# Performance work log

Hardware: AMD Instinct MI355X
Metric: run time of the kernel (lower is better)

Reference implementation:

```python
import jax, jax.numpy as jnp
import numpy as np
import math

B, S, E, H = 2, 2048, 1024, 16
HD = E // H          # head_dim = 64
HX = 64              # helix_dim
P = HX // 2          # helix pairs = 32

def setup_inputs() -> dict:
    key = jax.random.key(0)
    ks = jax.random.split(key, 12)
    sc = 0.02
    return {
        "x":    jax.random.normal(ks[0], (B, S, E), dtype=jnp.float32),
        "Wq":   jax.random.normal(ks[1], (E, E), dtype=jnp.float32) * sc,
        "bq":   jnp.zeros((E,), dtype=jnp.float32),
        "Wk":   jax.random.normal(ks[2], (E, E), dtype=jnp.float32) * sc,
        "bk":   jnp.zeros((E,), dtype=jnp.float32),
        "Wv":   jax.random.normal(ks[3], (E, E), dtype=jnp.float32) * sc,
        "bv":   jnp.zeros((E,), dtype=jnp.float32),
        "Wo":   jax.random.normal(ks[4], (E, E), dtype=jnp.float32) * sc,
        "bo":   jnp.zeros((E,), dtype=jnp.float32),
        "Whel": jax.random.normal(ks[5], (H, HX, HD), dtype=jnp.float32) * sc,
        "bhel": jnp.zeros((H, HX), dtype=jnp.float32),
    }

def _l2norm(x, eps=1e-12):
    # torch F.normalize(p=2, dim=-1): x / max(||x||, eps)
    n = jnp.sqrt(jnp.sum(x * x, axis=-1, keepdims=True))
    return x / jnp.maximum(n, eps)

def _scramble(t):
    # faithful to torch: (B,S,2) -> transpose(1,2) -> reshape(B,S,2),
    # vectorized over (H,P): t is (B,H,P,S,2)
    b, h, p, s, _ = t.shape
    return jnp.swapaxes(t, -1, -2).reshape(b, h, p, s, 2)

def reference(x, Wq, bq, Wk, bk, Wv, bv, Wo, bo, Whel, bhel):
    b, s, e = x.shape
    h, hx, hd = Whel.shape
    p = hx // 2
    q = x @ Wq.T + bq
    k = x @ Wk.T + bk
    v = x @ Wv.T + bv
    qh = q.reshape(b, s, h, hd)
    kh = k.reshape(b, s, h, hd)
    # per-head helical projections: (B,S,H,HX)
    q_hel = jnp.einsum('bshd,hed->bshe', qh, Whel) + bhel
    k_hel = jnp.einsum('bshd,hed->bshe', kh, Whel) + bhel
    # split into 2D coords, normalize each pair: (B,H,P,S,2)
    qn = _l2norm(q_hel.reshape(b, s, h, p, 2)).transpose(0, 2, 3, 1, 4)
    kn = _l2norm(k_hel.reshape(b, s, h, p, 2)).transpose(0, 2, 3, 1, 4)
    qn = _scramble(qn)
    kn = _scramble(kn)
    # helical similarity averaged over pairs: (B,H,S,S)
    helical = jnp.einsum('bhpsc,bhptc->bhst', qn, kn) / p
    # standard scaled dot-product scores
    dot = jnp.einsum('bshd,bthd->bhst', qh, kh) / math.sqrt(hd)
    alpha = 0.5
    attn = jax.nn.softmax(alpha * dot + (1.0 - alpha) * helical, axis=-1)
    vh = v.reshape(b, s, h, hd)
    out = jnp.einsum('bhst,bthd->bshd', attn, vh).reshape(b, s, e)
    return out @ Wo.T + bo
```

## Files before the change

### kernel.cpp

```cpp
#include <hip/hip_runtime.h>
#include <hip/hip_bf16.h>


typedef unsigned short u16;
typedef unsigned int u32;
typedef __attribute__((ext_vector_type(8))) __bf16 bf16x8;
typedef __attribute__((ext_vector_type(4))) float f32x4;
typedef __attribute__((ext_vector_type(16))) float f32x16;

union BFrag { u32 u[4]; bf16x8 b; };

__device__ __forceinline__ u16 f2b(float f) {
  u32 u = __float_as_uint(f);
  u32 r = (u + 0x7fffu + ((u >> 16) & 1u)) >> 16;
  return (u16)r;
}
__device__ __forceinline__ float b2f(u16 h) {
  return __uint_as_float(((u32)h) << 16);
}

__device__ __forceinline__ f32x4 mfma16(bf16x8 a, bf16x8 b, f32x4 c) {
  return __builtin_amdgcn_mfma_f32_16x16x32_bf16(a, b, c, 0, 0, 0);
}
__device__ __forceinline__ f32x16 mfma32(bf16x8 a, bf16x8 b, f32x16 c) {
  return __builtin_amdgcn_mfma_f32_32x32x16_bf16(a, b, c, 0, 0, 0);
}

__device__ __forceinline__ void gld16(void* lds, const void* g) {
  __builtin_amdgcn_global_load_lds(
      (const __attribute__((address_space(1))) unsigned int*)g,
      (__attribute__((address_space(3))) unsigned int*)lds, 16, 0, 0);
}

__device__ __forceinline__ void pl32swap(u32& a, u32& b, int l5) {
#if __has_builtin(__builtin_amdgcn_permlane32_swap)
  typedef unsigned int u32x2v __attribute__((ext_vector_type(2)));
  u32x2v r = __builtin_amdgcn_permlane32_swap(a, b, false, false);
  a = r[0];
  b = r[1];
#else
  u32 ea = __shfl_xor((int)a, 32);
  u32 eb = __shfl_xor((int)b, 32);
  u32 na = l5 ? eb : a;
  u32 nb = l5 ? b : ea;
  a = na;
  b = nb;
#endif
}

#define LOG2E 1.4426950408889634f

__global__ __launch_bounds__(256) void cast_kernel(
    const float* __restrict__ x,  const float* __restrict__ wq,
    const float* __restrict__ wk, const float* __restrict__ wv,
    const float* __restrict__ wo, const float* __restrict__ whel,
    u16* __restrict__ xb, u16* __restrict__ wb, u16* __restrict__ wob,
    u16* __restrict__ whb) {
  long long q = (long long)blockIdx.x * 256 + threadIdx.x;
  const float* s; u16* d; long long base;
  if (q < 1048576)      { s = x;    d = xb;            base = 0; }
  else if (q < 1310720) { s = wq;   d = wb;            base = 1048576; }
  else if (q < 1572864) { s = wk;   d = wb + 1048576;  base = 1310720; }
  else if (q < 1835008) { s = wv;   d = wb + 2097152;  base = 1572864; }
  else if (q < 2097152) { s = wo;   d = wob;           base = 1835008; }
  else                  { s = whel; d = whb;           base = 2097152; }
  long long e = (q - base) * 4;
  float4 v = *(const float4*)(s + e);
  ushort4 o;
  o.x = f2b(v.x); o.y = f2b(v.y); o.z = f2b(v.z); o.w = f2b(v.w);
  *(ushort4*)(d + e) = o;
}

__global__ __launch_bounds__(256, 3) void qkv_gemm(
    const u16* __restrict__ xb, const u16* __restrict__ wb,
    const float* __restrict__ bq, const float* __restrict__ bk,
    const float* __restrict__ bv, const u16* __restrict__ whb,
    const float* __restrict__ bhel,
    u16* __restrict__ Qcat, u16* __restrict__ Kcat, u16* __restrict__ vt) {
  union SM {
    struct { u16 Al[2][128][32]; u16 Bl[2][128][32]; u16 T[64][136]; } m;
    struct { u16 Th[4][32][72]; u16 Hs[2][128][64]; } e;
  };
  __shared__ SM sm;
  const int nt = blockIdx.x, mt = blockIdx.y;
  const int which = nt >> 3;
  const int n0 = (nt & 7) << 7;
  const int m0 = mt << 7;
  const int tid = threadIdx.x;
  const int wave = tid >> 6, lane = tid & 63;
  const int g = lane >> 4, c15 = lane & 15;
  const int wm = wave & 1, wn = wave >> 1;
  const u16* Wp = wb + (long long)which * (1024 * 1024) + n0 * 1024;
  const u16* Ap = xb + m0 * 1024;
  const int srow = (wave * 64 + lane) >> 2;
  const int scol = (lane & 3) << 3;

  f32x4 acc[4][4];
#pragma unroll
  for (int i = 0; i < 4; i++)
#pragma unroll
    for (int j = 0; j < 4; j++) acc[i][j] = f32x4{0.f, 0.f, 0.f, 0.f};

  gld16(&sm.m.Al[0][srow][scol],      Ap + srow * 1024 + scol);
  gld16(&sm.m.Al[0][64 + srow][scol], Ap + (64 + srow) * 1024 + scol);
  gld16(&sm.m.Bl[0][srow][scol],      Wp + srow * 1024 + scol);
  gld16(&sm.m.Bl[0][64 + srow][scol], Wp + (64 + srow) * 1024 + scol);

  for (int k0 = 0; k0 < 1024; k0 += 32) {
    const int c = (k0 >> 5) & 1;
    __syncthreads();
    if (k0 + 32 < 1024) {
      const int kn = k0 + 32;
      gld16(&sm.m.Al[c ^ 1][srow][scol],      Ap + srow * 1024 + kn + scol);
      gld16(&sm.m.Al[c ^ 1][64 + srow][scol],
            Ap + (64 + srow) * 1024 + kn + scol);
      gld16(&sm.m.Bl[c ^ 1][srow][scol],      Wp + srow * 1024 + kn + scol);
      gld16(&sm.m.Bl[c ^ 1][64 + srow][scol],
            Wp + (64 + srow) * 1024 + kn + scol);
    }
    bf16x8 a[4], b[4];
#pragma unroll
    for (int i = 0; i < 4; i++)
      a[i] = *(const bf16x8*)&sm.m.Al[c][wm * 64 + i * 16 + c15][g * 8];
#pragma unroll
    for (int j = 0; j < 4; j++)
      b[j] = *(const bf16x8*)&sm.m.Bl[c][wn * 64 + j * 16 + c15][g * 8];
#pragma unroll
    for (int i = 0; i < 4; i++)
#pragma unroll
      for (int j = 0; j < 4; j++) acc[i][j] = mfma16(a[i], b[j], acc[i][j]);
  }

  if (which == 2) {
#pragma unroll
    for (int half = 0; half < 2; ++half) {
      __syncthreads();
      if (wn == half) {
#pragma unroll
        for (int i = 0; i < 4; i++)
#pragma unroll
          for (int j = 0; j < 4; j++)
#pragma unroll
            for (int r = 0; r < 4; r++) {
              int nloc = j * 16 + c15;
              int mloc = wm * 64 + i * 16 + g * 4 + r;
              float v = acc[i][j][r] + bv[n0 + half * 64 + nloc];
              sm.m.T[nloc][mloc] = f2b(v);
            }
      }
      __syncthreads();
#pragma unroll
      for (int it = 0; it < 4; ++it) {
        int idx = it * 256 + tid;
        int row = idx >> 4;
        int cm = (idx & 15) * 8;
        int col = n0 + half * 64 + row;
        int hh = col >> 6, dd = col & 63;
        int m = m0 + cm;
        int bb2 = m >> 11, s = m & 2047;
        *(uint4*)&vt[(((bb2 * 16 + hh) * 64) + dd) * 2048 + s] =
            *(const uint4*)&sm.m.T[row][cm];
      }
    }
    return;
  }

  const float* bias = (which == 0) ? bq : bk;
  const float fold = (which == 0) ? (0.0625f * LOG2E) : 1.0f;
  const float osc  = (which == 0) ? (0.125f * LOG2E) : 0.125f;
  const int h0 = n0 >> 6;
  const int hsel = h0 + wn;
  u16* Dst = ((which == 0) ? Qcat : Kcat);

  bf16x8 wf[2][4];
#pragma unroll
  for (int kh = 0; kh < 2; ++kh)
#pragma unroll
    for (int nf = 0; nf < 4; ++nf)
      wf[kh][nf] = *(const bf16x8*)(whb + hsel * 4096 + (nf * 16 + c15) * 64 +
                                    kh * 32 + g * 8);

  __syncthreads();
  const int bb2 = m0 >> 11;
  const int ubase = (m0 & 2047) >> 1;

#pragma unroll
  for (int half = 0; half < 2; ++half) {
#pragma unroll
    for (int i2 = 0; i2 < 2; ++i2) {
      int i = half * 2 + i2;
#pragma unroll
      for (int j = 0; j < 4; ++j)
#pragma unroll
        for (int r = 0; r < 4; ++r) {
          int row = m0 + wm * 64 + i * 16 + g * 4 + r;
          int col = n0 + wn * 64 + j * 16 + c15;
          float vraw = acc[i][j][r] + bias[col];
          int bb = row >> 11, s = row & 2047;
          int d = col & 63;
          Dst[(((long long)(bb * 16 + hsel) * 2048) + s) * 128 + d] =
              f2b(vraw * fold);
          sm.e.Th[wave][i2 * 16 + g * 4 + r][j * 16 + c15] = f2b(vraw);
        }
    }
    f32x4 hacc[2][4];
#pragma unroll
    for (int mf = 0; mf < 2; ++mf)
#pragma unroll
      for (int nf = 0; nf < 4; ++nf) hacc[mf][nf] = f32x4{0.f, 0.f, 0.f, 0.f};
#pragma unroll
    for (int kh = 0; kh < 2; ++kh) {
      bf16x8 a0 = *(const bf16x8*)&sm.e.Th[wave][c15][kh * 32 + g * 8];
      bf16x8 a1 = *(const bf16x8*)&sm.e.Th[wave][16 + c15][kh * 32 + g * 8];
#pragma unroll
      for (int nf = 0; nf < 4; ++nf) {
        hacc[0][nf] = mfma16(a0, wf[kh][nf], hacc[0][nf]);
        hacc[1][nf] = mfma16(a1, wf[kh][nf], hacc[1][nf]);
      }
    }
#pragma unroll
    for (int mf = 0; mf < 2; ++mf)
#pragma unroll
      for (int nf = 0; nf < 4; ++nf)
#pragma unroll
        for (int r = 0; r < 4; ++r) {
          int e = nf * 16 + c15;
          float v = hacc[mf][nf][r] + bhel[hsel * 64 + e];
          float pp = __shfl_xor(v, 1);
          float nn = sqrtf(v * v + pp * pp);
          float o = v / fmaxf(nn, 1e-12f) * osc;
          int tl = wm * 64 + half * 32 + mf * 16 + g * 4 + r;
          sm.e.Hs[wn][(e & 1) * 64 + (tl >> 1)][(e & ~1) | (tl & 1)] = f2b(o);
        }
  }
  __syncthreads();
#pragma unroll
  for (int it = 0; it < 8; ++it) {
    int idx = it * 256 + tid;
    int hh = idx >> 10;
    int hr = (idx >> 3) & 127;
    int ck = idx & 7;
    int coord = hr >> 6, ul = hr & 63;
    int row_out = coord * 1024 + ubase + ul;
    *(uint4*)&Dst[(((long long)(bb2 * 16 + h0 + hh) * 2048) + row_out) * 128 +
                  64 + ck * 8] = *(const uint4*)&sm.e.Hs[hh][hr][ck * 8];
  }
}

__global__ __launch_bounds__(512, 4) void attn_kernel(
    const u16* __restrict__ Qcat, const u16* __restrict__ Kcat,
    const u16* __restrict__ vt, u16* __restrict__ AO) {
  __shared__ u16 Kl[2][64][128];
  __shared__ u16 Vl[2][64][64];
  __shared__ float denl[2][128];
  const int bh = blockIdx.x, qt = blockIdx.y;
  const int bb = bh >> 4, h = bh & 15;
  const int q0 = qt << 7;
  const int tid = threadIdx.x;
  const int w = tid >> 6, lane = tid & 63;
  const int wq = w & 3, wt = w >> 2;
  const int l31 = lane & 31, l5 = lane >> 5;
  const u16* Qb = Qcat + (long long)bh * (2048 * 128);
  const u16* Kb = Kcat + (long long)bh * (2048 * 128);
  const u16* Vb = vt + (long long)bh * (64 * 2048);

  bf16x8 qf[8];
  {
    const u16* qrow = Qb + (q0 + 32 * wq + l31) * 128 + l5 * 8;
#pragma unroll
    for (int ks = 0; ks < 8; ++ks) qf[ks] = *(const bf16x8*)(qrow + ks * 16);
  }

  const int ll = tid;
  const int krow0 = ll >> 4;
  const int kp = ll & 15;
  const int ksrc0 = (kp & 8) | ((kp & 7) ^ (krow0 & 7));
  const int krow1 = 32 + krow0;
  const int ksrc1 = (kp & 8) | ((kp & 7) ^ (krow1 & 7));
  const int vd = ll >> 3;
  const int vsrc = (ll & 7) ^ (vd & 7);

  gld16(((u16*)Kl[0]) + ll * 8,        Kb + krow0 * 128 + ksrc0 * 8);
  gld16(((u16*)Kl[0]) + 4096 + ll * 8, Kb + krow1 * 128 + ksrc1 * 8);
  gld16(((u16*)Vl[0]) + ll * 8,        Vb + vd * 2048 + vsrc * 8);

  f32x16 accO0, accO1;
#pragma unroll
  for (int i = 0; i < 16; ++i) { accO0[i] = 0.f; accO1[i] = 0.f; }
  float den = 0.f;

  const int krow = 32 * wt + l31;
  const int kr7 = krow & 7;

  for (int t = 0; t < 32; ++t) {
    const int cur = t & 1;
    __syncthreads();
    if (t + 1 < 32) {
      const int t1 = (t + 1) << 6;
      u16* Kd = (u16*)Kl[cur ^ 1];
      gld16(Kd + ll * 8,        Kb + (t1 + krow0) * 128 + ksrc0 * 8);
      gld16(Kd + 4096 + ll * 8, Kb + (t1 + krow1) * 128 + ksrc1 * 8);
      gld16(((u16*)Vl[cur ^ 1]) + ll * 8, Vb + vd * 2048 + t1 + vsrc * 8);
    }

    f32x16 accS;
#pragma unroll
    for (int i = 0; i < 16; ++i) accS[i] = 0.f;
#pragma unroll
    for (int ks = 0; ks < 8; ++ks) {
      int lc = 2 * ks + l5;
      int p = (lc & 8) | ((lc & 7) ^ kr7);
      bf16x8 ak = *(const bf16x8*)&Kl[cur][krow][p * 8];
      accS = mfma32(ak, qf[ks], accS);
    }

    u32 D0[2], D1[2], D2[2], D3[2];
#pragma unroll
    for (int rr = 0; rr < 4; ++rr) {
      float p0 = __builtin_amdgcn_exp2f(accS[4 * rr + 0]);
      float p1 = __builtin_amdgcn_exp2f(accS[4 * rr + 1]);
      float p2 = __builtin_amdgcn_exp2f(accS[4 * rr + 2]);
      float p3 = __builtin_amdgcn_exp2f(accS[4 * rr + 3]);
      den += (p0 + p1) + (p2 + p3);
      u32 lo = __builtin_amdgcn_perm(__float_as_uint(p1), __float_as_uint(p0),
                                     0x07060302u);
      u32 hi = __builtin_amdgcn_perm(__float_as_uint(p3), __float_as_uint(p2),
                                     0x07060302u);
      if (rr == 0) { D0[0] = lo; D0[1] = hi; }
      else if (rr == 1) { D1[0] = lo; D1[1] = hi; }
      else if (rr == 2) { D2[0] = lo; D2[1] = hi; }
      else { D3[0] = lo; D3[1] = hi; }
    }
    BFrag A0, A1;
    A0.u[0] = D0[0]; A0.u[2] = D1[0]; pl32swap(A0.u[0], A0.u[2], l5);
    A0.u[1] = D0[1]; A0.u[3] = D1[1]; pl32swap(A0.u[1], A0.u[3], l5);
    A1.u[0] = D2[0]; A1.u[2] = D3[0]; pl32swap(A1.u[0], A1.u[2], l5);
    A1.u[1] = D2[1]; A1.u[3] = D3[1]; pl32swap(A1.u[1], A1.u[3], l5);

#pragma unroll
    for (int dq = 0; dq < 2; ++dq) {
      int d = 32 * dq + l31;
      int d7 = d & 7;
#pragma unroll
      for (int ks = 0; ks < 2; ++ks) {
        int lc = 4 * wt + 2 * ks + l5;
        bf16x8 bvf = *(const bf16x8*)&Vl[cur][d][((lc ^ d7) & 7) * 8];
        if (dq == 0) accO0 = mfma32(ks ? A1.b : A0.b, bvf, accO0);
        else         accO1 = mfma32(ks ? A1.b : A0.b, bvf, accO1);
      }
    }
  }

  den += __shfl_xor(den, 32);
  if (lane < 32) denl[wt][32 * wq + lane] = den;
  __syncthreads();

  float* S = (float*)Kl;
  if (wt == 1) {
#pragma unroll
    for (int r = 0; r < 16; ++r) {
      int qr = (r & 3) + 8 * (r >> 2) + 4 * l5;
      S[(wq * 32 + qr) * 64 + l31] = accO0[r];
      S[(wq * 32 + qr) * 64 + 32 + l31] = accO1[r];
    }
  }
  __syncthreads();
  if (wt == 0) {
#pragma unroll
    for (int r = 0; r < 16; ++r) {
      int qr = (r & 3) + 8 * (r >> 2) + 4 * l5;
      int ql = 32 * wq + qr;
      float inv = 1.0f / (denl[0][ql] + denl[1][ql]);
      float o0 = (accO0[r] + S[(wq * 32 + qr) * 64 + l31]) * inv;
      float o1 = (accO1[r] + S[(wq * 32 + qr) * 64 + 32 + l31]) * inv;
      long long base = ((long long)(bb * 2048 + q0 + ql) * 1024) + h * 64;
      AO[base + l31] = f2b(o0);
      AO[base + 32 + l31] = f2b(o1);
    }
  }
}

__global__ __launch_bounds__(256, 2) void out_gemm(
    const u16* __restrict__ AO, const u16* __restrict__ wob,
    const float* __restrict__ bo, float* __restrict__ out) {
  __shared__ u16 Al[2][128][32];
  __shared__ u16 Bl[2][64][32];
  const int n0 = blockIdx.x << 6;
  const int m0 = blockIdx.y << 7;
  const int tid = threadIdx.x;
  const int wave = tid >> 6, lane = tid & 63;
  const int g = lane >> 4, c15 = lane & 15;
  const int wm = wave & 1, wn = wave >> 1;
  const u16* Wp = wob + n0 * 1024;
  const u16* Ap = AO + m0 * 1024;
  const int srow = tid >> 2;
  const int scol = (tid & 3) << 3;

  f32x4 acc[4][2];
#pragma unroll
  for (int i = 0; i < 4; i++)
#pragma unroll
    for (int j = 0; j < 2; j++) acc[i][j] = f32x4{0.f, 0.f, 0.f, 0.f};

  gld16(&Al[0][srow][scol],      Ap + srow * 1024 + scol);
  gld16(&Al[0][64 + srow][scol], Ap + (64 + srow) * 1024 + scol);
  gld16(&Bl[0][srow][scol],      Wp + srow * 1024 + scol);

  for (int k0 = 0; k0 < 1024; k0 += 32) {
    const int c = (k0 >> 5) & 1;
    __syncthreads();
    if (k0 + 32 < 1024) {
      const int kn = k0 + 32;
      gld16(&Al[c ^ 1][srow][scol],      Ap + srow * 1024 + kn + scol);
      gld16(&Al[c ^ 1][64 + srow][scol], Ap + (64 + srow) * 1024 + kn + scol);
      gld16(&Bl[c ^ 1][srow][scol],      Wp + srow * 1024 + kn + scol);
    }
    bf16x8 a[4], b[2];
#pragma unroll
    for (int i = 0; i < 4; i++)
      a[i] = *(const bf16x8*)&Al[c][wm * 64 + i * 16 + c15][g * 8];
#pragma unroll
    for (int j = 0; j < 2; j++)
      b[j] = *(const bf16x8*)&Bl[c][wn * 32 + j * 16 + c15][g * 8];
#pragma unroll
    for (int i = 0; i < 4; i++)
#pragma unroll
      for (int j = 0; j < 2; j++) acc[i][j] = mfma16(a[i], b[j], acc[i][j]);
  }
#pragma unroll
  for (int i = 0; i < 4; i++)
#pragma unroll
    for (int j = 0; j < 2; j++)
#pragma unroll
      for (int r = 0; r < 4; r++) {
        int row = m0 + wm * 64 + i * 16 + g * 4 + r;
        int col = n0 + wn * 32 + j * 16 + c15;
        out[row * 1024 + col] = acc[i][j][r] + bo[col];
      }
}

extern "C" void kernel_launch(void* const* d_in, const int* in_sizes, int n_in,
                              void* d_out, int out_size, void* d_ws,
                              size_t ws_size, hipStream_t stream) {
  const float* x    = (const float*)d_in[0];
  const float* Wq   = (const float*)d_in[1];
  const float* bq   = (const float*)d_in[2];
  const float* Wk   = (const float*)d_in[3];
  const float* bk   = (const float*)d_in[4];
  const float* Wv   = (const float*)d_in[5];
  const float* bv   = (const float*)d_in[6];
  const float* Wo   = (const float*)d_in[7];
  const float* bo   = (const float*)d_in[8];
  const float* Whel = (const float*)d_in[9];
  const float* bhel = (const float*)d_in[10];
  float* out = (float*)d_out;

  char* ws = (char*)d_ws;
  u16* xb   = (u16*)(ws + 0);
  u16* wb   = (u16*)(ws + 8388608);
  u16* wob  = (u16*)(ws + 14680064);
  u16* whb  = (u16*)(ws + 16777216);
  u16* Qcat = (u16*)(ws + 16908288);
  u16* Kcat = (u16*)(ws + 33685504);
  u16* vt   = (u16*)(ws + 50462720);
  u16* AO   = (u16*)(ws + 58851328);

  cast_kernel<<<dim3(8256), dim3(256), 0, stream>>>(x, Wq, Wk, Wv, Wo, Whel,
                                                    xb, wb, wob, whb);
  qkv_gemm<<<dim3(24, 32), dim3(256), 0, stream>>>(xb, wb, bq, bk, bv, whb,
                                                   bhel, Qcat, Kcat, vt);
  attn_kernel<<<dim3(32, 16), dim3(512), 0, stream>>>(Qcat, Kcat, vt, AO);
  out_gemm<<<dim3(16, 32), dim3(256), 0, stream>>>(AO, wob, bo, out);
}
```

Before: 228.7 us.

## Double query rows per attention block to reuse K/V tiles across two Q fragments

```diff
diff --git a/kernel.cpp b/kernel.cpp
--- a/kernel.cpp
+++ b/kernel.cpp
@@ -247,15 +247,15 @@
   }
 }
 
-__global__ __launch_bounds__(512, 4) void attn_kernel(
+__global__ __launch_bounds__(512, 2) void attn_kernel(
     const u16* __restrict__ Qcat, const u16* __restrict__ Kcat,
     const u16* __restrict__ vt, u16* __restrict__ AO) {
   __shared__ u16 Kl[2][64][128];
   __shared__ u16 Vl[2][64][64];
-  __shared__ float denl[2][128];
+  __shared__ float denl[2][256];
   const int bh = blockIdx.x, qt = blockIdx.y;
   const int bb = bh >> 4, h = bh & 15;
-  const int q0 = qt << 7;
+  const int q0 = qt << 8;
   const int tid = threadIdx.x;
   const int w = tid >> 6, lane = tid & 63;
   const int wq = w & 3, wt = w >> 2;
@@ -264,11 +264,15 @@
   const u16* Kb = Kcat + (long long)bh * (2048 * 128);
   const u16* Vb = vt + (long long)bh * (64 * 2048);
 
-  bf16x8 qf[8];
+  bf16x8 qf0[8], qf1[8];
   {
-    const u16* qrow = Qb + (q0 + 32 * wq + l31) * 128 + l5 * 8;
-#pragma unroll
-    for (int ks = 0; ks < 8; ++ks) qf[ks] = *(const bf16x8*)(qrow + ks * 16);
+    const u16* qrow0 = Qb + (q0 + 64 * wq + l31) * 128 + l5 * 8;
+    const u16* qrow1 = qrow0 + 32 * 128;
+#pragma unroll
+    for (int ks = 0; ks < 8; ++ks) {
+      qf0[ks] = *(const bf16x8*)(qrow0 + ks * 16);
+      qf1[ks] = *(const bf16x8*)(qrow1 + ks * 16);
+    }
   }
 
   const int ll = tid;
@@ -284,10 +288,12 @@
   gld16(((u16*)Kl[0]) + 4096 + ll * 8, Kb + krow1 * 128 + ksrc1 * 8);
   gld16(((u16*)Vl[0]) + ll * 8,        Vb + vd * 2048 + vsrc * 8);
 
-  f32x16 accO0, accO1;
-#pragma unroll
-  for (int i = 0; i < 16; ++i) { accO0[i] = 0.f; accO1[i] = 0.f; }
-  float den = 0.f;
+  f32x16 accO00, accO01, accO10, accO11;
+#pragma unroll
+  for (int i = 0; i < 16; ++i) {
+    accO00[i] = 0.f; accO01[i] = 0.f; accO10[i] = 0.f; accO11[i] = 0.f;
+  }
+  float den0 = 0.f, den1 = 0.f;
 
   const int krow = 32 * wt + l31;
   const int kr7 = krow & 7;
@@ -303,39 +309,65 @@
       gld16(((u16*)Vl[cur ^ 1]) + ll * 8, Vb + vd * 2048 + t1 + vsrc * 8);
     }
 
-    f32x16 accS;
-#pragma unroll
-    for (int i = 0; i < 16; ++i) accS[i] = 0.f;
+    f32x16 accS0, accS1;
+#pragma unroll
+    for (int i = 0; i < 16; ++i) { accS0[i] = 0.f; accS1[i] = 0.f; }
 #pragma unroll
     for (int ks = 0; ks < 8; ++ks) {
       int lc = 2 * ks + l5;
       int p = (lc & 8) | ((lc & 7) ^ kr7);
       bf16x8 ak = *(const bf16x8*)&Kl[cur][krow][p * 8];
-      accS = mfma32(ak, qf[ks], accS);
-    }
-
-    u32 D0[2], D1[2], D2[2], D3[2];
-#pragma unroll
-    for (int rr = 0; rr < 4; ++rr) {
-      float p0 = __builtin_amdgcn_exp2f(accS[4 * rr + 0]);
-      float p1 = __builtin_amdgcn_exp2f(accS[4 * rr + 1]);
-      float p2 = __builtin_amdgcn_exp2f(accS[4 * rr + 2]);
-      float p3 = __builtin_amdgcn_exp2f(accS[4 * rr + 3]);
-      den += (p0 + p1) + (p2 + p3);
-      u32 lo = __builtin_amdgcn_perm(__float_as_uint(p1), __float_as_uint(p0),
-                                     0x07060302u);
-      u32 hi = __builtin_amdgcn_perm(__float_as_uint(p3), __float_as_uint(p2),
-                                     0x07060302u);
-      if (rr == 0) { D0[0] = lo; D0[1] = hi; }
-      else if (rr == 1) { D1[0] = lo; D1[1] = hi; }
-      else if (rr == 2) { D2[0] = lo; D2[1] = hi; }
-      else { D3[0] = lo; D3[1] = hi; }
-    }
-    BFrag A0, A1;
-    A0.u[0] = D0[0]; A0.u[2] = D1[0]; pl32swap(A0.u[0], A0.u[2], l5);
-    A0.u[1] = D0[1]; A0.u[3] = D1[1]; pl32swap(A0.u[1], A0.u[3], l5);
-    A1.u[0] = D2[0]; A1.u[2] = D3[0]; pl32swap(A1.u[0], A1.u[2], l5);
-    A1.u[1] = D2[1]; A1.u[3] = D3[1]; pl32swap(A1.u[1], A1.u[3], l5);
+      accS0 = mfma32(ak, qf0[ks], accS0);
+      accS1 = mfma32(ak, qf1[ks], accS1);
+    }
+
+    BFrag A0q0, A1q0, A0q1, A1q1;
+    {
+      u32 D0[2], D1[2], D2[2], D3[2];
+#pragma unroll
+      for (int rr = 0; rr < 4; ++rr) {
+        float p0 = __builtin_amdgcn_exp2f(accS0[4 * rr + 0]);
+        float p1 = __builtin_amdgcn_exp2f(accS0[4 * rr + 1]);
+        float p2 = __builtin_amdgcn_exp2f(accS0[4 * rr + 2]);
+        float p3 = __builtin_amdgcn_exp2f(accS0[4 * rr + 3]);
+        den0 += (p0 + p1) + (p2 + p3);
+        u32 lo = __builtin_amdgcn_perm(__float_as_uint(p1),
+                                       __float_as_uint(p0), 0x07060302u);
+        u32 hi = __builtin_amdgcn_perm(__float_as_uint(p3),
+                                       __float_as_uint(p2), 0x07060302u);
+        if (rr == 0) { D0[0] = lo; D0[1] = hi; }
+        else if (rr == 1) { D1[0] = lo; D1[1] = hi; }
+        else if (rr == 2) { D2[0] = lo; D2[1] = hi; }
+        else { D3[0] = lo; D3[1] = hi; }
+      }
+      A0q0.u[0] = D0[0]; A0q0.u[2] = D1[0]; pl32swap(A0q0.u[0], A0q0.u[2], l5);
+      A0q0.u[1] = D0[1]; A0q0.u[3] = D1[1]; pl32swap(A0q0.u[1], A0q0.u[3], l5);
+      A1q0.u[0] = D2[0]; A1q0.u[2] = D3[0]; pl32swap(A1q0.u[0], A1q0.u[2], l5);
+      A1q0.u[1] = D2[1]; A1q0.u[3] = D3[1]; pl32swap(A1q0.u[1], A1q0.u[3], l5);
+    }
+    {
+      u32 D0[2], D1[2], D2[2], D3[2];
+#pragma unroll
+      for (int rr = 0; rr < 4; ++rr) {
+        float p0 = __builtin_amdgcn_exp2f(accS1[4 * rr + 0]);
+        float p1 = __builtin_amdgcn_exp2f(accS1[4 * rr + 1]);
+        float p2 = __builtin_amdgcn_exp2f(accS1[4 * rr + 2]);
+        float p3 = __builtin_amdgcn_exp2f(accS1[4 * rr + 3]);
+        den1 += (p0 + p1) + (p2 + p3);
+        u32 lo = __builtin_amdgcn_perm(__float_as_uint(p1),
+                                       __float_as_uint(p0), 0x07060302u);
+        u32 hi = __builtin_amdgcn_perm(__float_as_uint(p3),
+                                       __float_as_uint(p2), 0x07060302u);
+        if (rr == 0) { D0[0] = lo; D0[1] = hi; }
+        else if (rr == 1) { D1[0] = lo; D1[1] = hi; }
+        else if (rr == 2) { D2[0] = lo; D2[1] = hi; }
+        else { D3[0] = lo; D3[1] = hi; }
+      }
+      A0q1.u[0] = D0[0]; A0q1.u[2] = D1[0]; pl32swap(A0q1.u[0], A0q1.u[2], l5);
+      A0q1.u[1] = D0[1]; A0q1.u[3] = D1[1]; pl32swap(A0q1.u[1], A0q1.u[3], l5);
+      A1q1.u[0] = D2[0]; A1q1.u[2] = D3[0]; pl32swap(A1q1.u[0], A1q1.u[2], l5);
+      A1q1.u[1] = D2[1]; A1q1.u[3] = D3[1]; pl32swap(A1q1.u[1], A1q1.u[3], l5);
+    }
 
 #pragma unroll
     for (int dq = 0; dq < 2; ++dq) {
@@ -345,37 +377,54 @@
       for (int ks = 0; ks < 2; ++ks) {
         int lc = 4 * wt + 2 * ks + l5;
         bf16x8 bvf = *(const bf16x8*)&Vl[cur][d][((lc ^ d7) & 7) * 8];
-        if (dq == 0) accO0 = mfma32(ks ? A1.b : A0.b, bvf, accO0);
-        else         accO1 = mfma32(ks ? A1.b : A0.b, bvf, accO1);
-      }
-    }
-  }
-
-  den += __shfl_xor(den, 32);
-  if (lane < 32) denl[wt][32 * wq + lane] = den;
-  __syncthreads();
-
-  float* S = (float*)Kl;
-  if (wt == 1) {
-#pragma unroll
-    for (int r = 0; r < 16; ++r) {
-      int qr = (r & 3) + 8 * (r >> 2) + 4 * l5;
-      S[(wq * 32 + qr) * 64 + l31] = accO0[r];
-      S[(wq * 32 + qr) * 64 + 32 + l31] = accO1[r];
-    }
-  }
-  __syncthreads();
-  if (wt == 0) {
-#pragma unroll
-    for (int r = 0; r < 16; ++r) {
-      int qr = (r & 3) + 8 * (r >> 2) + 4 * l5;
-      int ql = 32 * wq + qr;
-      float inv = 1.0f / (denl[0][ql] + denl[1][ql]);
-      float o0 = (accO0[r] + S[(wq * 32 + qr) * 64 + l31]) * inv;
-      float o1 = (accO1[r] + S[(wq * 32 + qr) * 64 + 32 + l31]) * inv;
-      long long base = ((long long)(bb * 2048 + q0 + ql) * 1024) + h * 64;
-      AO[base + l31] = f2b(o0);
-      AO[base + 32 + l31] = f2b(o1);
+        if (dq == 0) {
+          accO00 = mfma32(ks ? A1q0.b : A0q0.b, bvf, accO00);
+          accO10 = mfma32(ks ? A1q1.b : A0q1.b, bvf, accO10);
+        } else {
+          accO01 = mfma32(ks ? A1q0.b : A0q0.b, bvf, accO01);
+          accO11 = mfma32(ks ? A1q1.b : A0q1.b, bvf, accO11);
+        }
+      }
+    }
+  }
+
+  den0 += __shfl_xor(den0, 32);
+  den1 += __shfl_xor(den1, 32);
+  if (lane < 32) {
+    denl[wt][64 * wq + lane] = den0;
+    denl[wt][64 * wq + 32 + lane] = den1;
+  }
+
+  float* Ssc = (float*)Kl;
+#pragma unroll
+  for (int dq = 0; dq < 2; ++dq) {
+    __syncthreads();
+    if (wt == 1) {
+#pragma unroll
+      for (int qs = 0; qs < 2; ++qs)
+#pragma unroll
+        for (int r = 0; r < 16; ++r) {
+          int qr = (r & 3) + 8 * (r >> 2) + 4 * l5;
+          float v = dq ? (qs ? accO11[r] : accO01[r])
+                       : (qs ? accO10[r] : accO00[r]);
+          Ssc[(wq * 64 + qs * 32 + qr) * 32 + l31] = v;
+        }
+    }
+    __syncthreads();
+    if (wt == 0) {
+#pragma unroll
+      for (int qs = 0; qs < 2; ++qs)
+#pragma unroll
+        for (int r = 0; r < 16; ++r) {
+          int qr = (r & 3) + 8 * (r >> 2) + 4 * l5;
+          int ql = 64 * wq + 32 * qs + qr;
+          float inv = 1.0f / (denl[0][ql] + denl[1][ql]);
+          float mine = dq ? (qs ? accO11[r] : accO01[r])
+                          : (qs ? accO10[r] : accO00[r]);
+          float o = (mine + Ssc[(wq * 64 + qs * 32 + qr) * 32 + l31]) * inv;
+          long long base = ((long long)(bb * 2048 + q0 + ql) * 1024) + h * 64;
+          AO[base + 32 * dq + l31] = f2b(o);
+        }
     }
   }
 }
@@ -469,6 +518,6 @@
                                                     xb, wb, wob, whb);
   qkv_gemm<<<dim3(24, 32), dim3(256), 0, stream>>>(xb, wb, bq, bk, bv, whb,
                                                    bhel, Qcat, Kcat, vt);
-  attn_kernel<<<dim3(32, 16), dim3(512), 0, stream>>>(Qcat, Kcat, vt, AO);
+  attn_kernel<<<dim3(32, 8), dim3(512), 0, stream>>>(Qcat, Kcat, vt, AO);
   out_gemm<<<dim3(16, 32), dim3(256), 0, stream>>>(AO, wob, bo, out);
 }
```

Measured after the change: 235.2 us. +2.9%, slower.

## Triple-buffer K/V and GEMM tiles with partial vmcnt waits

Applied to the files above, without the earlier changes.

```diff
diff --git a/kernel.cpp b/kernel.cpp
--- a/kernel.cpp
+++ b/kernel.cpp
@@ -49,6 +49,14 @@
 }
 
 #define LOG2E 1.4426950408889634f
+
+#define PIPE_BARRIER(N)                                         \
+  do {                                                          \
+    __builtin_amdgcn_sched_barrier(0);                          \
+    asm volatile("s_waitcnt vmcnt(" #N ")" ::: "memory");       \
+    __builtin_amdgcn_s_barrier();                               \
+    __builtin_amdgcn_sched_barrier(0);                          \
+  } while (0)
 
 __global__ __launch_bounds__(256) void cast_kernel(
     const float* __restrict__ x,  const float* __restrict__ wq,
@@ -250,8 +258,8 @@
 __global__ __launch_bounds__(512, 4) void attn_kernel(
     const u16* __restrict__ Qcat, const u16* __restrict__ Kcat,
     const u16* __restrict__ vt, u16* __restrict__ AO) {
-  __shared__ u16 Kl[2][64][128];
-  __shared__ u16 Vl[2][64][64];
+  __shared__ u16 Kl[3][64][128];
+  __shared__ u16 Vl[3][64][64];
   __shared__ float denl[2][128];
   const int bh = blockIdx.x, qt = blockIdx.y;
   const int bb = bh >> 4, h = bh & 15;
@@ -283,6 +291,9 @@
   gld16(((u16*)Kl[0]) + ll * 8,        Kb + krow0 * 128 + ksrc0 * 8);
   gld16(((u16*)Kl[0]) + 4096 + ll * 8, Kb + krow1 * 128 + ksrc1 * 8);
   gld16(((u16*)Vl[0]) + ll * 8,        Vb + vd * 2048 + vsrc * 8);
+  gld16(((u16*)Kl[1]) + ll * 8,        Kb + (64 + krow0) * 128 + ksrc0 * 8);
+  gld16(((u16*)Kl[1]) + 4096 + ll * 8, Kb + (64 + krow1) * 128 + ksrc1 * 8);
+  gld16(((u16*)Vl[1]) + ll * 8,        Vb + vd * 2048 + 64 + vsrc * 8);
 
   f32x16 accO0, accO1;
 #pragma unroll
@@ -292,15 +303,16 @@
   const int krow = 32 * wt + l31;
   const int kr7 = krow & 7;
 
+  int cur = 0;
   for (int t = 0; t < 32; ++t) {
-    const int cur = t & 1;
-    __syncthreads();
-    if (t + 1 < 32) {
-      const int t1 = (t + 1) << 6;
-      u16* Kd = (u16*)Kl[cur ^ 1];
-      gld16(Kd + ll * 8,        Kb + (t1 + krow0) * 128 + ksrc0 * 8);
-      gld16(Kd + 4096 + ll * 8, Kb + (t1 + krow1) * 128 + ksrc1 * 8);
-      gld16(((u16*)Vl[cur ^ 1]) + ll * 8, Vb + vd * 2048 + t1 + vsrc * 8);
+    if (t < 31) { PIPE_BARRIER(3); } else { PIPE_BARRIER(0); }
+    if (t + 2 < 32) {
+      const int pf = (cur >= 1) ? cur - 1 : 2;
+      const int t2 = (t + 2) << 6;
+      u16* Kd = (u16*)Kl[pf];
+      gld16(Kd + ll * 8,        Kb + (t2 + krow0) * 128 + ksrc0 * 8);
+      gld16(Kd + 4096 + ll * 8, Kb + (t2 + krow1) * 128 + ksrc1 * 8);
+      gld16(((u16*)Vl[pf]) + ll * 8, Vb + vd * 2048 + t2 + vsrc * 8);
     }
 
     f32x16 accS;
@@ -349,6 +361,7 @@
         else         accO1 = mfma32(ks ? A1.b : A0.b, bvf, accO1);
       }
     }
+    cur = (cur == 2) ? 0 : cur + 1;
   }
 
   den += __shfl_xor(den, 32);
@@ -383,8 +396,8 @@
 __global__ __launch_bounds__(256, 2) void out_gemm(
     const u16* __restrict__ AO, const u16* __restrict__ wob,
     const float* __restrict__ bo, float* __restrict__ out) {
-  __shared__ u16 Al[2][128][32];
-  __shared__ u16 Bl[2][64][32];
+  __shared__ u16 Al[3][128][32];
+  __shared__ u16 Bl[3][64][32];
   const int n0 = blockIdx.x << 6;
   const int m0 = blockIdx.y << 7;
   const int tid = threadIdx.x;
@@ -405,27 +418,32 @@
   gld16(&Al[0][srow][scol],      Ap + srow * 1024 + scol);
   gld16(&Al[0][64 + srow][scol], Ap + (64 + srow) * 1024 + scol);
   gld16(&Bl[0][srow][scol],      Wp + srow * 1024 + scol);
-
-  for (int k0 = 0; k0 < 1024; k0 += 32) {
-    const int c = (k0 >> 5) & 1;
-    __syncthreads();
-    if (k0 + 32 < 1024) {
-      const int kn = k0 + 32;
-      gld16(&Al[c ^ 1][srow][scol],      Ap + srow * 1024 + kn + scol);
-      gld16(&Al[c ^ 1][64 + srow][scol], Ap + (64 + srow) * 1024 + kn + scol);
-      gld16(&Bl[c ^ 1][srow][scol],      Wp + srow * 1024 + kn + scol);
+  gld16(&Al[1][srow][scol],      Ap + srow * 1024 + 32 + scol);
+  gld16(&Al[1][64 + srow][scol], Ap + (64 + srow) * 1024 + 32 + scol);
+  gld16(&Bl[1][srow][scol],      Wp + srow * 1024 + 32 + scol);
+
+  int cur = 0;
+  for (int it = 0; it < 32; ++it) {
+    if (it < 31) { PIPE_BARRIER(3); } else { PIPE_BARRIER(0); }
+    if (it + 2 < 32) {
+      const int pf = (cur >= 1) ? cur - 1 : 2;
+      const int kn = (it + 2) << 5;
+      gld16(&Al[pf][srow][scol],      Ap + srow * 1024 + kn + scol);
+      gld16(&Al[pf][64 + srow][scol], Ap + (64 + srow) * 1024 + kn + scol);
+      gld16(&Bl[pf][srow][scol],      Wp + srow * 1024 + kn + scol);
     }
     bf16x8 a[4], b[2];
 #pragma unroll
     for (int i = 0; i < 4; i++)
-      a[i] = *(const bf16x8*)&Al[c][wm * 64 + i * 16 + c15][g * 8];
+      a[i] = *(const bf16x8*)&Al[cur][wm * 64 + i * 16 + c15][g * 8];
 #pragma unroll
     for (int j = 0; j < 2; j++)
-      b[j] = *(const bf16x8*)&Bl[c][wn * 32 + j * 16 + c15][g * 8];
+      b[j] = *(const bf16x8*)&Bl[cur][wn * 32 + j * 16 + c15][g * 8];
 #pragma unroll
     for (int i = 0; i < 4; i++)
 #pragma unroll
       for (int j = 0; j < 2; j++) acc[i][j] = mfma16(a[i], b[j], acc[i][j]);
+    cur = (cur == 2) ? 0 : cur + 1;
   }
 #pragma unroll
   for (int i = 0; i < 4; i++)
```

Result: faster. 222.9 us (-2.5%).
